# Optimization experiments

Measured on AMD Instinct MI355X. Metric: run time of the kernel, lower is better.

The kernel has to match this reference:

```python
import jax, jax.numpy as jnp
import numpy as np

NEG = -9e15
ALPHA = 0.2  # LeakyReLU negative slope


def _gat_layer(x, W, a, mask):
    # x: [N, Fin], W: [Fin, Fout], a: [2*Fout, 1], mask: [N, N] bool
    h = x @ W                                  # [N, Fout]
    F = h.shape[1]
    # additive attention score: identical math to cat([h_i, h_j]) @ a
    f1 = h @ a[:F, 0]                          # [N]
    f2 = h @ a[F:, 0]                          # [N]
    e = jax.nn.leaky_relu(f1[:, None] + f2[None, :], ALPHA)  # [N, N]
    e = jnp.where(mask, e, NEG)
    attn = jax.nn.softmax(e, axis=1)           # dropout is identity in eval mode
    return attn @ h                            # [N, Fout]


def setup_inputs() -> dict:
    key = jax.random.key(0)
    ks = jax.random.split(key, 6)
    N, Fin, H, Fh, Fo = 4096, 256, 8, 64, 64
    features = jax.random.normal(ks[0], (N, Fin), dtype=jnp.float32)
    adj = jax.random.randint(ks[1], (N, N), 0, 2).astype(jnp.float32)
    W_heads = jax.random.normal(ks[2], (H, Fin, Fh), dtype=jnp.float32) * 0.1
    a_heads = jax.random.normal(ks[3], (H, 2 * Fh, 1), dtype=jnp.float32) * 0.1
    W_out = jax.random.normal(ks[4], (H * Fh, Fo), dtype=jnp.float32) * 0.1
    a_out = jax.random.normal(ks[5], (2 * Fo, 1), dtype=jnp.float32) * 0.1
    return {"features": features, "adj": adj, "W_heads": W_heads,
            "a_heads": a_heads, "W_out": W_out, "a_out": a_out}


def reference(features, adj, W_heads, a_heads, W_out, a_out):
    mask = adj > 0
    H = W_heads.shape[0]
    # loop over the small fixed set of heads (keeps peak memory at one NxN matrix)
    heads = [jax.nn.elu(_gat_layer(features, W_heads[i], a_heads[i], mask))
             for i in range(H)]
    x = jnp.concatenate(heads, axis=1)         # [N, H*Fh]
    return _gat_layer(x, W_out, a_out, mask)   # concat=False -> no elu
```

## Files before the change

### kernel.cpp

```cpp
#include <hip/hip_runtime.h>
#include <hip/hip_bf16.h>

#define N_NODES 4096
#define LOG2E 1.44269504088896340736f
#define JT 128

typedef __attribute__((ext_vector_type(8))) short bf16x8;
typedef __attribute__((ext_vector_type(4))) short bf16x4;
typedef __attribute__((ext_vector_type(4))) float f32x4;
typedef __attribute__((ext_vector_type(16))) float f32x16;

static __device__ __forceinline__ ushort f2bf(float x) {
    union { float f; unsigned u; } v; v.f = x;
    unsigned u = v.u;
    return (ushort)((u + 0x7FFFu + ((u >> 16) & 1u)) >> 16);
}

__global__ __launch_bounds__(256) void k_pack_mask(const float* __restrict__ adj,
                                                   unsigned* __restrict__ maskw) {
    int idx = blockIdx.x * 256 + threadIdx.x;
    int row = idx >> 7, w = idx & 127;
    const float4* ap = (const float4*)(adj + (size_t)row * N_NODES + w * 32);
    unsigned bits = 0;
#pragma unroll
    for (int q = 0; q < 8; ++q) {
        float4 v = ap[q];
        bits |= (v.x > 0.f ? 1u : 0u) << (q * 4 + 0);
        bits |= (v.y > 0.f ? 1u : 0u) << (q * 4 + 1);
        bits |= (v.z > 0.f ? 1u : 0u) << (q * 4 + 2);
        bits |= (v.w > 0.f ? 1u : 0u) << (q * 4 + 3);
    }
    maskw[idx] = bits;
}

__global__ void k_prep_w(const float* __restrict__ W, ushort* __restrict__ Wh,
                         ushort* __restrict__ Wl, int kshift, int total) {
    int idx = blockIdx.x * 256 + threadIdx.x;
    if (idx >= total) return;
    int K = 1 << kshift;
    int n = idx & 63;
    int k = (idx >> 6) & (K - 1);
    int h = idx >> (6 + kshift);
    float v = W[idx];
    ushort hi = f2bf(v);
    union { unsigned u; float f; } hv; hv.u = ((unsigned)hi) << 16;
    ushort lo = f2bf(v - hv.f);
    size_t dst = ((size_t)h * 64 + n) * K + k;
    Wh[dst] = hi; Wl[dst] = lo;
}

__global__ __launch_bounds__(512) void k_gemm_h(const float* __restrict__ X,
        const ushort* __restrict__ Wh, const ushort* __restrict__ Wl,
        const float* __restrict__ a,
        ushort* __restrict__ Ht, float* __restrict__ Rc,
        float* __restrict__ Tc, ushort* __restrict__ G2b, int K) {
    int head = blockIdx.y;
    int t = threadIdx.x, wave = t >> 6, lane = t & 63;
    int c = lane & 15, g = lane >> 4;
    int i0 = blockIdx.x * 16;
    int kq = K >> 3;
    int kbeg = wave * kq;
    const float* xrow = X + (size_t)(i0 + c) * K;
    f32x4 acc[4] = {};
    for (int k0 = kbeg; k0 < kbeg + kq; k0 += 32) {
        const float4* xp = (const float4*)(xrow + k0 + g * 8);
        float4 xa = xp[0], xb = xp[1];
        float xs[8] = {xa.x, xa.y, xa.z, xa.w, xb.x, xb.y, xb.z, xb.w};
        union { ushort s[8]; bf16x8 v; } ah, al;
#pragma unroll
        for (int e = 0; e < 8; ++e) {
            ushort hb = f2bf(xs[e]);
            ah.s[e] = hb;
            union { unsigned u; float f; } hv; hv.u = ((unsigned)hb) << 16;
            al.s[e] = f2bf(xs[e] - hv.f);
        }
#pragma unroll
        for (int nt = 0; nt < 4; ++nt) {
            size_t boff = ((size_t)head * 64 + nt * 16 + c) * K + k0 + g * 8;
            bf16x8 bh = *(const bf16x8*)(Wh + boff);
            bf16x8 bl = *(const bf16x8*)(Wl + boff);
            acc[nt] = __builtin_amdgcn_mfma_f32_16x16x32_bf16(ah.v, bh, acc[nt], 0, 0, 0);
            acc[nt] = __builtin_amdgcn_mfma_f32_16x16x32_bf16(al.v, bh, acc[nt], 0, 0, 0);
            acc[nt] = __builtin_amdgcn_mfma_f32_16x16x32_bf16(ah.v, bl, acc[nt], 0, 0, 0);
        }
    }
    __shared__ float red[8][64][17];
#pragma unroll
    for (int nt = 0; nt < 4; ++nt)
#pragma unroll
        for (int r = 0; r < 4; ++r)
            red[wave][lane][nt * 4 + r] = acc[nt][r];
    __syncthreads();
    if (wave != 0) return;
#pragma unroll
    for (int nt = 0; nt < 4; ++nt)
#pragma unroll
        for (int r = 0; r < 4; ++r) {
            float s = 0.f;
#pragma unroll
            for (int w = 0; w < 8; ++w) s += red[w][lane][nt * 4 + r];
            acc[nt][r] = s;
        }
    float a1v[4], a2v[4];
#pragma unroll
    for (int nt = 0; nt < 4; ++nt) {
        a1v[nt] = a[head * 128 + nt * 16 + c];
        a2v[nt] = a[head * 128 + 64 + nt * 16 + c];
    }
    float G2f[4];
#pragma unroll
    for (int r = 0; r < 4; ++r) {
        float f1 = 0.f, f2 = 0.f;
#pragma unroll
        for (int nt = 0; nt < 4; ++nt) {
            f1 = __builtin_fmaf(acc[nt][r], a1v[nt], f1);
            f2 = __builtin_fmaf(acc[nt][r], a2v[nt], f2);
        }
#pragma unroll
        for (int o = 1; o < 16; o <<= 1) {
            f1 += __shfl_xor(f1, o);
            f2 += __shfl_xor(f2, o);
        }
        float g2 = __builtin_amdgcn_exp2f(0.2f * LOG2E * f2);
        G2f[r] = g2;
        if (c == 0) {
            int i = i0 + g * 4 + r;
            Rc [head * N_NODES + i] = __builtin_amdgcn_exp2f(-0.8f * LOG2E * f1);
            Tc [head * N_NODES + i] = __builtin_amdgcn_exp2f( 0.8f * LOG2E * f2);
            G2b[head * N_NODES + i] = f2bf(g2);
        }
    }
#pragma unroll
    for (int nt = 0; nt < 4; ++nt) {
        union { ushort s[4]; bf16x4 v; } pk;
#pragma unroll
        for (int r = 0; r < 4; ++r) pk.s[r] = f2bf(acc[nt][r] * G2f[r]);
        *(bf16x4*)(Ht + ((size_t)head * 64 + nt * 16 + c) * N_NODES + i0 + g * 4) = pk.v;
    }
}

__global__ __launch_bounds__(256)
__attribute__((amdgpu_waves_per_eu(4, 8)))
void k_attn(const ushort* __restrict__ Ht,
        const float* __restrict__ Rc, const float* __restrict__ Tc,
        const ushort* __restrict__ G2b, const unsigned* __restrict__ maskw,
        float* __restrict__ accP, float* __restrict__ Zp, int JS) {
    int rb = blockIdx.x, js = blockIdx.y, head = blockIdx.z;
    int t = threadIdx.x, wave = t >> 6, lane = t & 63;
    int r32 = lane & 31, half = lane >> 5;
    int i0b = rb * 128;
    int i0w = i0b + wave * 32;
    int irow = i0w + r32;
    int jcount = N_NODES / JS;
    int j0 = js * jcount;
    int ntiles = jcount / JT;
    const float R = Rc[head * N_NODES + irow];

    __shared__ ushort Hs[2][64 * JT];
    __shared__ unsigned Ms[2][512];
    __shared__ float Ts[2][JT];
    __shared__ ushort G2s[2][JT];

    int nH = (wave * 4) * 4 + (lane >> 4);
    const ushort* gspH[4];
#pragma unroll
    for (int s = 0; s < 4; ++s) {
        int n = nH + s * 4;
        gspH[s] = Ht + ((size_t)head * 64 + n) * N_NODES + j0
                + (((lane & 15) ^ (n & 7)) << 3);
    }
    const unsigned* msrc[8];
#pragma unroll
    for (int s = 0; s < 8; ++s)
        msrc[s] = maskw + (size_t)(i0b + s * 16 + (lane >> 2)) * 128 + (j0 >> 5) + (lane & 3);
    const float*  tsrc = Tc  + (size_t)head * N_NODES + j0 + lane;
    const ushort* gsrc = G2b + (size_t)head * N_NODES + j0 + lane * 2;

    auto stage = [&](int b, int tile) {
        int go = tile * JT;
#pragma unroll
        for (int s = 0; s < 4; ++s)
            __builtin_amdgcn_global_load_lds((const unsigned*)(gspH[s] + go),
                    (unsigned*)&Hs[b][(wave * 4 + s) * 512], 16, 0, 0);
        if (wave == 0) {
#pragma unroll
            for (int s = 0; s < 8; ++s)
                __builtin_amdgcn_global_load_lds((const unsigned*)(msrc[s] + tile * 4),
                        (unsigned*)&Ms[b][s * 64], 4, 0, 0);
        } else if (wave == 1) {
#pragma unroll
            for (int s = 0; s < 2; ++s)
                __builtin_amdgcn_global_load_lds((const unsigned*)(tsrc + go + s * 64),
                        (unsigned*)&Ts[b][s * 64], 4, 0, 0);
        } else if (wave == 2) {
            __builtin_amdgcn_global_load_lds((const unsigned*)(gsrc + go),
                    (unsigned*)&G2s[b][0], 4, 0, 0);
        }
    };

    f32x16 acc0 = {}, acc1 = {}, acc2 = {};

    stage(0, 0);
    int buf = 0;
    for (int tile = 0; tile < ntiles; ++tile) {
        if (tile + 1 < ntiles) {
            stage(buf ^ 1, tile + 1);
            if (wave == 0)      asm volatile("s_waitcnt vmcnt(12)");
            else if (wave == 1) asm volatile("s_waitcnt vmcnt(6)");
            else if (wave == 2) asm volatile("s_waitcnt vmcnt(5)");
            else                asm volatile("s_waitcnt vmcnt(4)");
        } else {
            asm volatile("s_waitcnt vmcnt(0)");
        }
        __builtin_amdgcn_s_barrier();

        const char* hb = (const char*)&Hs[buf][0];
#pragma unroll
        for (int itr = 0; itr < JT / 16; ++itr) {
            unsigned phys = (unsigned)(((itr * 2 + half) ^ (r32 & 7)) << 4);
            bf16x8 b0 = *(const bf16x8*)(hb + r32 * 256 + phys);
            bf16x8 b1 = *(const bf16x8*)(hb + (32 + r32) * 256 + phys);
            bf16x8 bg = *(const bf16x8*)(&G2s[buf][itr * 16 + half * 8]);
            unsigned mword = Ms[buf][(wave * 32 + r32) * 4 + (itr >> 1)];
            unsigned mshift = mword >> ((itr & 1) * 16 + half * 8);
            const float* tp = &Ts[buf][itr * 16 + half * 8];
            float4 ta = *(const float4*)tp;
            float4 tb = *(const float4*)(tp + 4);
            float tv[8] = {ta.x, ta.y, ta.z, ta.w, tb.x, tb.y, tb.z, tb.w};
            float p[8];
#pragma unroll
            for (int e = 0; e < 8; ++e) {
                int sm = (int)(mshift << (31 - e)) >> 31;
                float pe = fmaxf(tv[e], R);
                union { float f; int i; } pv; pv.f = pe;
                pv.i &= sm;
                p[e] = pv.f;
            }
            union { unsigned w[4]; bf16x8 v; } pa;
#pragma unroll
            for (int q = 0; q < 4; ++q)
                asm("v_cvt_pk_bf16_f32 %0, %1, %2"
                    : "=v"(pa.w[q]) : "v"(p[2 * q]), "v"(p[2 * q + 1]));
            acc0 = __builtin_amdgcn_mfma_f32_32x32x16_bf16(pa.v, b0, acc0, 0, 0, 0);
            acc1 = __builtin_amdgcn_mfma_f32_32x32x16_bf16(pa.v, b1, acc1, 0, 0, 0);
            acc2 = __builtin_amdgcn_mfma_f32_32x32x16_bf16(pa.v, bg, acc2, 0, 0, 0);
        }
        __builtin_amdgcn_s_barrier();
        buf ^= 1;
    }
    int slice = head * JS + js;
    if (r32 == 0) {
#pragma unroll
        for (int reg = 0; reg < 16; ++reg) {
            int drow = (reg & 3) + 8 * (reg >> 2) + 4 * half;
            Zp[(size_t)slice * N_NODES + i0w + drow] = acc2[reg];
        }
    }
    float* ap = accP + ((size_t)slice * N_NODES + i0w) * 64;
#pragma unroll
    for (int reg = 0; reg < 16; ++reg) {
        int drow = (reg & 3) + 8 * (reg >> 2) + 4 * half;
        ap[drow * 64 + r32] = acc0[reg];
        ap[drow * 64 + 32 + r32] = acc1[reg];
    }
}

__global__ __launch_bounds__(256) void k_combine1(const float* __restrict__ accP,
        const float* __restrict__ Zp, float* __restrict__ x2, int JS) {
    int idx = blockIdx.x * 256 + threadIdx.x;
    int n = idx & 63, i = (idx >> 6) & 4095, h = idx >> 18;
    float s = 0.f, z = 0.f;
    for (int j = 0; j < JS; ++j) {
        int sl = h * JS + j;
        s += accP[((size_t)sl * N_NODES + i) * 64 + n];
        z += Zp[(size_t)sl * N_NODES + i];
    }
    float v = s / z;
    v = v > 0.f ? v : (__builtin_amdgcn_exp2f(v * LOG2E) - 1.f);
    x2[(size_t)i * 512 + h * 64 + n] = v;
}

__global__ __launch_bounds__(256) void k_combine2(const float* __restrict__ accP,
        const float* __restrict__ Zp, float* __restrict__ out, int JS) {
    int idx = blockIdx.x * 256 + threadIdx.x;
    int n = idx & 63, i = idx >> 6;
    float s = 0.f, z = 0.f;
    for (int j = 0; j < JS; ++j) {
        s += accP[((size_t)j * N_NODES + i) * 64 + n];
        z += Zp[(size_t)j * N_NODES + i];
    }
    out[idx] = s / z;
}

extern "C" void kernel_launch(void* const* d_in, const int* in_sizes, int n_in,
                              void* d_out, int out_size, void* d_ws, size_t ws_size,
                              hipStream_t stream) {
    const float* features = (const float*)d_in[0];
    const float* adj      = (const float*)d_in[1];
    const float* W_heads  = (const float*)d_in[2];
    const float* a_heads  = (const float*)d_in[3];
    const float* W_out    = (const float*)d_in[4];
    const float* a_out    = (const float*)d_in[5];
    float* out = (float*)d_out;

    int JS1, JS2;
    if (ws_size >= 51800000)      { JS1 = 4; JS2 = 32; }
    else if (ws_size >= 34800000) { JS1 = 2; JS2 = 16; }
    else                          { JS1 = 1; JS2 = 8;  }
    int slices = (8 * JS1 > JS2) ? 8 * JS1 : JS2;

    char* ws = (char*)d_ws;
    size_t off = 0;
    auto alloc = [&](size_t bytes) -> void* {
        void* p = ws + off; off = (off + bytes + 255) & ~(size_t)255; return p;
    };
    unsigned* maskw = (unsigned*)alloc((size_t)N_NODES * 128 * 4);
    ushort* Ht1 = (ushort*)alloc((size_t)8 * 64 * N_NODES * 2);
    ushort* Ht2 = (ushort*)alloc((size_t)64 * N_NODES * 2);
    float* Rc1  = (float*)alloc((size_t)8 * N_NODES * 4);
    float* Tc1  = (float*)alloc((size_t)8 * N_NODES * 4);
    ushort* G2b1 = (ushort*)alloc((size_t)8 * N_NODES * 2);
    float* Rc2  = (float*)alloc((size_t)N_NODES * 4);
    float* Tc2  = (float*)alloc((size_t)N_NODES * 4);
    ushort* G2b2 = (ushort*)alloc((size_t)N_NODES * 2);
    ushort* Wh1 = (ushort*)alloc((size_t)8 * 64 * 256 * 2);
    ushort* Wl1 = (ushort*)alloc((size_t)8 * 64 * 256 * 2);
    ushort* Wh2 = (ushort*)alloc((size_t)64 * 512 * 2);
    ushort* Wl2 = (ushort*)alloc((size_t)64 * 512 * 2);
    float* x2   = (float*)alloc((size_t)N_NODES * 512 * 4);
    float* accP = (float*)alloc((size_t)slices * N_NODES * 64 * 4);
    float* Zp   = (float*)alloc((size_t)slices * N_NODES * 4);

    hipLaunchKernelGGL(k_pack_mask, dim3(N_NODES * 128 / 256), dim3(256), 0, stream, adj, maskw);
    hipLaunchKernelGGL(k_prep_w, dim3((8 * 256 * 64 + 255) / 256), dim3(256), 0, stream,
                       W_heads, Wh1, Wl1, 8, 8 * 256 * 64);
    hipLaunchKernelGGL(k_prep_w, dim3((512 * 64 + 255) / 256), dim3(256), 0, stream,
                       W_out, Wh2, Wl2, 9, 512 * 64);
    hipLaunchKernelGGL(k_gemm_h, dim3(N_NODES / 16, 8), dim3(512), 0, stream,
                       features, Wh1, Wl1, a_heads, Ht1, Rc1, Tc1, G2b1, 256);
    hipLaunchKernelGGL(k_attn, dim3(32, JS1, 8), dim3(256), 0, stream,
                       Ht1, Rc1, Tc1, G2b1, maskw, accP, Zp, JS1);
    hipLaunchKernelGGL(k_combine1, dim3(8 * N_NODES * 64 / 256), dim3(256), 0, stream,
                       accP, Zp, x2, JS1);
    hipLaunchKernelGGL(k_gemm_h, dim3(N_NODES / 16, 1), dim3(512), 0, stream,
                       x2, Wh2, Wl2, a_out, Ht2, Rc2, Tc2, G2b2, 512);
    hipLaunchKernelGGL(k_attn, dim3(32, JS2, 1), dim3(256), 0, stream,
                       Ht2, Rc2, Tc2, G2b2, maskw, accP, Zp, JS2);
    hipLaunchKernelGGL(k_combine2, dim3(N_NODES * 64 / 256), dim3(256), 0, stream,
                       accP, Zp, out, JS2);
}
```

Before: 130.0 us.

## Fuse layer-1 combine into second GEMM and merge prologue kernels

Replaces the separate combine1 kernel and second k_gemm_h launch with k_gemm2. It reduces the per-head split partials, normalises, applies ELU and feeds the result straight into the MFMA GEMM, with a cross-wave LDS reduction. This removes the x2 round trip through global memory, and the lower workspace thresholds let the wider splits fit more often. The mask-packing and weight-split kernels are merged into one prologue launch to cut launch overhead. The attention kernel now loads the mask words as one vector load per tile and caps waves_per_eu at 4, which gives the compiler more registers but may lower occupancy.

```diff
diff --git a/kernel.cpp b/kernel.cpp
--- a/kernel.cpp
+++ b/kernel.cpp
@@ -16,37 +16,40 @@
     return (ushort)((u + 0x7FFFu + ((u >> 16) & 1u)) >> 16);
 }
 
-__global__ __launch_bounds__(256) void k_pack_mask(const float* __restrict__ adj,
-                                                   unsigned* __restrict__ maskw) {
-    int idx = blockIdx.x * 256 + threadIdx.x;
-    int row = idx >> 7, w = idx & 127;
-    const float4* ap = (const float4*)(adj + (size_t)row * N_NODES + w * 32);
-    unsigned bits = 0;
-#pragma unroll
-    for (int q = 0; q < 8; ++q) {
-        float4 v = ap[q];
-        bits |= (v.x > 0.f ? 1u : 0u) << (q * 4 + 0);
-        bits |= (v.y > 0.f ? 1u : 0u) << (q * 4 + 1);
-        bits |= (v.z > 0.f ? 1u : 0u) << (q * 4 + 2);
-        bits |= (v.w > 0.f ? 1u : 0u) << (q * 4 + 3);
-    }
-    maskw[idx] = bits;
-}
-
-__global__ void k_prep_w(const float* __restrict__ W, ushort* __restrict__ Wh,
-                         ushort* __restrict__ Wl, int kshift, int total) {
-    int idx = blockIdx.x * 256 + threadIdx.x;
-    if (idx >= total) return;
-    int K = 1 << kshift;
-    int n = idx & 63;
-    int k = (idx >> 6) & (K - 1);
-    int h = idx >> (6 + kshift);
-    float v = W[idx];
-    ushort hi = f2bf(v);
-    union { unsigned u; float f; } hv; hv.u = ((unsigned)hi) << 16;
-    ushort lo = f2bf(v - hv.f);
-    size_t dst = ((size_t)h * 64 + n) * K + k;
-    Wh[dst] = hi; Wl[dst] = lo;
+__global__ __launch_bounds__(256) void k_prologue(const float* __restrict__ adj,
+        unsigned* __restrict__ maskw,
+        const float* __restrict__ W1, ushort* __restrict__ Wh1, ushort* __restrict__ Wl1,
+        const float* __restrict__ W2, ushort* __restrict__ Wh2, ushort* __restrict__ Wl2) {
+    int b = blockIdx.x, t = threadIdx.x;
+    if (b < 2048) {
+        int idx = b * 256 + t;
+        int row = idx >> 7, w = idx & 127;
+        const float4* ap = (const float4*)(adj + (size_t)row * N_NODES + w * 32);
+        unsigned bits = 0;
+#pragma unroll
+        for (int q = 0; q < 8; ++q) {
+            float4 v = ap[q];
+            bits |= (v.x > 0.f ? 1u : 0u) << (q * 4 + 0);
+            bits |= (v.y > 0.f ? 1u : 0u) << (q * 4 + 1);
+            bits |= (v.z > 0.f ? 1u : 0u) << (q * 4 + 2);
+            bits |= (v.w > 0.f ? 1u : 0u) << (q * 4 + 3);
+        }
+        maskw[idx] = bits;
+    } else {
+        const float* W; ushort *Wh, *Wl; int idx, kshift;
+        if (b < 2560) { W = W1; Wh = Wh1; Wl = Wl1; idx = (b - 2048) * 256 + t; kshift = 8; }
+        else          { W = W2; Wh = Wh2; Wl = Wl2; idx = (b - 2560) * 256 + t; kshift = 9; }
+        int K = 1 << kshift;
+        int n = idx & 63;
+        int k = (idx >> 6) & (K - 1);
+        int h = idx >> (6 + kshift);
+        float v = W[idx];
+        ushort hi = f2bf(v);
+        union { unsigned u; float f; } hv; hv.u = ((unsigned)hi) << 16;
+        ushort lo = f2bf(v - hv.f);
+        size_t dst = ((size_t)h * 64 + n) * K + k;
+        Wh[dst] = hi; Wl[dst] = lo;
+    }
 }
 
 __global__ __launch_bounds__(512) void k_gemm_h(const float* __restrict__ X,
@@ -139,8 +142,112 @@
     }
 }
 
+__global__ __launch_bounds__(512) void k_gemm2(const float* __restrict__ accP,
+        const float* __restrict__ Zp, int JS1,
+        const ushort* __restrict__ Wh, const ushort* __restrict__ Wl,
+        const float* __restrict__ a,
+        ushort* __restrict__ Ht, float* __restrict__ Rc,
+        float* __restrict__ Tc, ushort* __restrict__ G2b) {
+    const int K = 512;
+    int t = threadIdx.x, wave = t >> 6, lane = t & 63;
+    int c = lane & 15, g = lane >> 4;
+    int i0 = blockIdx.x * 16;
+    int row = i0 + c;
+    int hx = wave;
+    float z = 0.f;
+    for (int js = 0; js < JS1; ++js)
+        z += Zp[(size_t)(hx * JS1 + js) * N_NODES + row];
+    float rz = 1.0f / z;
+    f32x4 acc[4] = {};
+#pragma unroll
+    for (int ki = 0; ki < 2; ++ki) {
+        int k0 = wave * 64 + ki * 32;
+        int n0 = ki * 32 + g * 8;
+        float s[8] = {};
+        for (int js = 0; js < JS1; ++js) {
+            const float* apn = accP + ((size_t)(hx * JS1 + js) * N_NODES + row) * 64 + n0;
+            float4 u0 = ((const float4*)apn)[0];
+            float4 u1 = ((const float4*)apn)[1];
+            s[0] += u0.x; s[1] += u0.y; s[2] += u0.z; s[3] += u0.w;
+            s[4] += u1.x; s[5] += u1.y; s[6] += u1.z; s[7] += u1.w;
+        }
+        union { ushort sh[8]; bf16x8 v; } ah, al;
+#pragma unroll
+        for (int e = 0; e < 8; ++e) {
+            float v = s[e] * rz;
+            v = v > 0.f ? v : (__builtin_amdgcn_exp2f(v * LOG2E) - 1.f);
+            ushort hb = f2bf(v);
+            ah.sh[e] = hb;
+            union { unsigned u; float f; } hv; hv.u = ((unsigned)hb) << 16;
+            al.sh[e] = f2bf(v - hv.f);
+        }
+#pragma unroll
+        for (int nt = 0; nt < 4; ++nt) {
+            size_t boff = ((size_t)(nt * 16 + c)) * K + k0 + g * 8;
+            bf16x8 bh = *(const bf16x8*)(Wh + boff);
+            bf16x8 bl = *(const bf16x8*)(Wl + boff);
+            acc[nt] = __builtin_amdgcn_mfma_f32_16x16x32_bf16(ah.v, bh, acc[nt], 0, 0, 0);
+            acc[nt] = __builtin_amdgcn_mfma_f32_16x16x32_bf16(al.v, bh, acc[nt], 0, 0, 0);
+            acc[nt] = __builtin_amdgcn_mfma_f32_16x16x32_bf16(ah.v, bl, acc[nt], 0, 0, 0);
+        }
+    }
+    __shared__ float red[8][64][17];
+#pragma unroll
+    for (int nt = 0; nt < 4; ++nt)
+#pragma unroll
+        for (int r = 0; r < 4; ++r)
+            red[wave][lane][nt * 4 + r] = acc[nt][r];
+    __syncthreads();
+    if (wave != 0) return;
+#pragma unroll
+    for (int nt = 0; nt < 4; ++nt)
+#pragma unroll
+        for (int r = 0; r < 4; ++r) {
+            float s = 0.f;
+#pragma unroll
+            for (int w = 0; w < 8; ++w) s += red[w][lane][nt * 4 + r];
+            acc[nt][r] = s;
+        }
+    float a1v[4], a2v[4];
+#pragma unroll
+    for (int nt = 0; nt < 4; ++nt) {
+        a1v[nt] = a[nt * 16 + c];
+        a2v[nt] = a[64 + nt * 16 + c];
+    }
+    float G2f[4];
+#pragma unroll
+    for (int r = 0; r < 4; ++r) {
+        float f1 = 0.f, f2 = 0.f;
+#pragma unroll
+        for (int nt = 0; nt < 4; ++nt) {
+            f1 = __builtin_fmaf(acc[nt][r], a1v[nt], f1);
+            f2 = __builtin_fmaf(acc[nt][r], a2v[nt], f2);
+        }
+#pragma unroll
+        for (int o = 1; o < 16; o <<= 1) {
+            f1 += __shfl_xor(f1, o);
+            f2 += __shfl_xor(f2, o);
+        }
+        float g2 = __builtin_amdgcn_exp2f(0.2f * LOG2E * f2);
+        G2f[r] = g2;
+        if (c == 0) {
+            int i = i0 + g * 4 + r;
+            Rc [i] = __builtin_amdgcn_exp2f(-0.8f * LOG2E * f1);
+            Tc [i] = __builtin_amdgcn_exp2f( 0.8f * LOG2E * f2);
+            G2b[i] = f2bf(g2);
+        }
+    }
+#pragma unroll
+    for (int nt = 0; nt < 4; ++nt) {
+        union { ushort s[4]; bf16x4 v; } pk;
+#pragma unroll
+        for (int r = 0; r < 4; ++r) pk.s[r] = f2bf(acc[nt][r] * G2f[r]);
+        *(bf16x4*)(Ht + ((size_t)(nt * 16 + c)) * N_NODES + i0 + g * 4) = pk.v;
+    }
+}
+
 __global__ __launch_bounds__(256)
-__attribute__((amdgpu_waves_per_eu(4, 8)))
+__attribute__((amdgpu_waves_per_eu(4, 4)))
 void k_attn(const ushort* __restrict__ Ht,
         const float* __restrict__ Rc, const float* __restrict__ Tc,
         const ushort* __restrict__ G2b, const unsigned* __restrict__ maskw,
@@ -215,13 +322,15 @@
         __builtin_amdgcn_s_barrier();
 
         const char* hb = (const char*)&Hs[buf][0];
+        union { uint4 v; unsigned w[4]; } mw;
+        mw.v = *(const uint4*)&Ms[buf][(wave * 32 + r32) * 4];
 #pragma unroll
         for (int itr = 0; itr < JT / 16; ++itr) {
             unsigned phys = (unsigned)(((itr * 2 + half) ^ (r32 & 7)) << 4);
             bf16x8 b0 = *(const bf16x8*)(hb + r32 * 256 + phys);
             bf16x8 b1 = *(const bf16x8*)(hb + (32 + r32) * 256 + phys);
             bf16x8 bg = *(const bf16x8*)(&G2s[buf][itr * 16 + half * 8]);
-            unsigned mword = Ms[buf][(wave * 32 + r32) * 4 + (itr >> 1)];
+            unsigned mword = mw.w[itr >> 1];
             unsigned mshift = mword >> ((itr & 1) * 16 + half * 8);
             const float* tp = &Ts[buf][itr * 16 + half * 8];
             float4 ta = *(const float4*)tp;
@@ -263,21 +372,6 @@
         ap[drow * 64 + r32] = acc0[reg];
         ap[drow * 64 + 32 + r32] = acc1[reg];
     }
-}
-
-__global__ __launch_bounds__(256) void k_combine1(const float* __restrict__ accP,
-        const float* __restrict__ Zp, float* __restrict__ x2, int JS) {
-    int idx = blockIdx.x * 256 + threadIdx.x;
-    int n = idx & 63, i = (idx >> 6) & 4095, h = idx >> 18;
-    float s = 0.f, z = 0.f;
-    for (int j = 0; j < JS; ++j) {
-        int sl = h * JS + j;
-        s += accP[((size_t)sl * N_NODES + i) * 64 + n];
-        z += Zp[(size_t)sl * N_NODES + i];
-    }
-    float v = s / z;
-    v = v > 0.f ? v : (__builtin_amdgcn_exp2f(v * LOG2E) - 1.f);
-    x2[(size_t)i * 512 + h * 64 + n] = v;
 }
 
 __global__ __launch_bounds__(256) void k_combine2(const float* __restrict__ accP,
@@ -304,8 +398,8 @@
     float* out = (float*)d_out;
 
     int JS1, JS2;
-    if (ws_size >= 51800000)      { JS1 = 4; JS2 = 32; }
-    else if (ws_size >= 34800000) { JS1 = 2; JS2 = 16; }
+    if (ws_size >= 43000000)      { JS1 = 4; JS2 = 32; }
+    else if (ws_size >= 26000000) { JS1 = 2; JS2 = 16; }
     else                          { JS1 = 1; JS2 = 8;  }
     int slices = (8 * JS1 > JS2) ? 8 * JS1 : JS2;
 
@@ -327,23 +421,17 @@
     ushort* Wl1 = (ushort*)alloc((size_t)8 * 64 * 256 * 2);
     ushort* Wh2 = (ushort*)alloc((size_t)64 * 512 * 2);
     ushort* Wl2 = (ushort*)alloc((size_t)64 * 512 * 2);
-    float* x2   = (float*)alloc((size_t)N_NODES * 512 * 4);
     float* accP = (float*)alloc((size_t)slices * N_NODES * 64 * 4);
     float* Zp   = (float*)alloc((size_t)slices * N_NODES * 4);
 
-    hipLaunchKernelGGL(k_pack_mask, dim3(N_NODES * 128 / 256), dim3(256), 0, stream, adj, maskw);
-    hipLaunchKernelGGL(k_prep_w, dim3((8 * 256 * 64 + 255) / 256), dim3(256), 0, stream,
-                       W_heads, Wh1, Wl1, 8, 8 * 256 * 64);
-    hipLaunchKernelGGL(k_prep_w, dim3((512 * 64 + 255) / 256), dim3(256), 0, stream,
-                       W_out, Wh2, Wl2, 9, 512 * 64);
+    hipLaunchKernelGGL(k_prologue, dim3(2688), dim3(256), 0, stream,
+                       adj, maskw, W_heads, Wh1, Wl1, W_out, Wh2, Wl2);
     hipLaunchKernelGGL(k_gemm_h, dim3(N_NODES / 16, 8), dim3(512), 0, stream,
                        features, Wh1, Wl1, a_heads, Ht1, Rc1, Tc1, G2b1, 256);
     hipLaunchKernelGGL(k_attn, dim3(32, JS1, 8), dim3(256), 0, stream,
                        Ht1, Rc1, Tc1, G2b1, maskw, accP, Zp, JS1);
-    hipLaunchKernelGGL(k_combine1, dim3(8 * N_NODES * 64 / 256), dim3(256), 0, stream,
-                       accP, Zp, x2, JS1);
-    hipLaunchKernelGGL(k_gemm_h, dim3(N_NODES / 16, 1), dim3(512), 0, stream,
-                       x2, Wh2, Wl2, a_out, Ht2, Rc2, Tc2, G2b2, 512);
+    hipLaunchKernelGGL(k_gemm2, dim3(N_NODES / 16), dim3(512), 0, stream,
+                       accP, Zp, JS1, Wh2, Wl2, a_out, Ht2, Rc2, Tc2, G2b2);
     hipLaunchKernelGGL(k_attn, dim3(32, JS2, 1), dim3(256), 0, stream,
                        Ht2, Rc2, Tc2, G2b2, maskw, accP, Zp, JS2);
     hipLaunchKernelGGL(k_combine2, dim3(N_NODES * 64 / 256), dim3(256), 0, stream,
```

Result: faster. 121.6 us (-6.5%).
